# Kernel tuning notes

Measured on AMD Instinct MI355X. Metric: run time of the kernel, lower is better.

Reference implementation:

```python
import jax, jax.numpy as jnp
import numpy as np

B, T, N_EMBED, HEAD = 512, 256, 384, 64
BLOCK = 256
SCALE = N_EMBED ** -0.5  # source scales by input-channel dim, not head_size


def setup_inputs() -> dict:
    key = jax.random.key(0)
    kx, kk, kq, kv = jax.random.split(key, 4)
    x = jax.random.normal(kx, (B, T, N_EMBED), dtype=jnp.float32)
    # torch Linear(n_embed, head_size, bias=False) weights, stored as (in, out)
    s = N_EMBED ** -0.5
    Wk = jax.random.normal(kk, (N_EMBED, HEAD), dtype=jnp.float32) * s
    Wq = jax.random.normal(kq, (N_EMBED, HEAD), dtype=jnp.float32) * s
    Wv = jax.random.normal(kv, (N_EMBED, HEAD), dtype=jnp.float32) * s
    return {"x": x, "Wk": Wk, "Wq": Wq, "Wv": Wv}


def reference(x, Wk, Wq, Wv):
    Bx, Tx, _ = x.shape
    K = jnp.einsum('btc,ch->bth', x, Wk)
    Q = jnp.einsum('btc,ch->bth', x, Wq)
    V = jnp.einsum('btc,ch->bth', x, Wv)
    scores = jnp.einsum('bth,bsh->bts', Q, K) * SCALE  # [B, T, T]
    causal = jnp.tril(jnp.ones((Tx, Tx), dtype=bool))
    scores = jnp.where(causal[None, :, :], scores, -jnp.inf)
    W = jax.nn.softmax(scores, axis=-1)
    # dropout is identity in eval mode (reference baseline is deterministic)
    out = jnp.einsum('bts,bsh->bth', W, V)
    return out
```

## Files before the change

kernel.cpp:

```cpp
#include <hip/hip_runtime.h>
#include <hip/hip_bf16.h>

#define B_  512
#define T_  256
#define C_  384
#define H_  64
#define SCALE_ 0.05103103630798287f

typedef float f32x4  __attribute__((ext_vector_type(4)));
typedef short bf16x8 __attribute__((ext_vector_type(8)));
typedef short bf16x4 __attribute__((ext_vector_type(4)));

__device__ __forceinline__ unsigned short f2bf(float f) {
    union { float f; unsigned u; } v; v.f = f;
    unsigned r = v.u + 0x7FFFu + ((v.u >> 16) & 1u);
    return (unsigned short)(r >> 16);
}

__device__ __forceinline__ unsigned cvt_pk_bf16(float lo, float hi) {
    unsigned r;
    asm("v_cvt_pk_bf16_f32 %0, %1, %2" : "=v"(r) : "v"(lo), "v"(hi));
    return r;
}

__device__ __forceinline__ int swz64(int row, int col) {
    return row * 64 + (((col >> 3) ^ (row & 7)) << 3) + (col & 7);
}

__global__ __launch_bounds__(1024, 4) void att_head_kernel(
    const float* __restrict__ x,  const float* __restrict__ Wk,
    const float* __restrict__ Wq, const float* __restrict__ Wv,
    float* __restrict__ out)
{
    __shared__ __align__(16) short smem[53760];
    short* const wst0 = smem;
    short* const wst1 = smem + 12288;
    short* const Ks   = smem;
    short* const Vt   = smem + 16384;
    short* const Pb   = smem + 33280;

    const int tid  = threadIdx.x;
    const int b    = blockIdx.x;
    const int w    = tid >> 6;
    const int lane = tid & 63;
    const int g    = lane >> 4;
    const int i    = lane & 15;
    const int rb   = 16 * w;

    const float* xb = x + (size_t)b * T_ * C_;
    const float* Wm[3] = { Wk, Wq, Wv };

    f32x4 accP[12];
    #pragma unroll
    for (int nb = 0; nb < 12; nb++) accP[nb] = f32x4{0.f, 0.f, 0.f, 0.f};

    const float* xrow = xb + (size_t)(rb + i) * C_ + g * 8;

    auto stageW = [&](int kc, short* buf) {
        #pragma unroll
        for (int m = 0; m < 3; m++) {
            const float* Wp = Wm[m] + (size_t)(kc + w * 4) * H_ + lane;
            bf16x4 pk;
            #pragma unroll
            for (int jj = 0; jj < 4; jj++) pk[jj] = (short)f2bf(Wp[jj * H_]);
            const int row = m * 64 + lane;
            const int k0  = w * 4;
            *(bf16x4*)&buf[row * 64 + (((k0 >> 3) ^ (row & 7)) << 3) + (k0 & 7)] = pk;
        }
    };

    float4 xr[2][4];
    #pragma unroll
    for (int ks = 0; ks < 2; ks++)
        #pragma unroll
        for (int h = 0; h < 2; h++)
            xr[0][ks * 2 + h] = *(const float4*)(xrow + ks * 32 + h * 4);
    stageW(0, wst0);
    asm volatile("s_waitcnt lgkmcnt(0)\n\ts_barrier" ::: "memory");

    #pragma unroll
    for (int j = 0; j < 6; j++) {
        const int par = j & 1;
        short* cur = par ? wst1 : wst0;
        if (j < 5) {
            #pragma unroll
            for (int ks = 0; ks < 2; ks++)
                #pragma unroll
                for (int h = 0; h < 2; h++)
                    xr[par ^ 1][ks * 2 + h] = *(const float4*)(xrow + (j + 1) * 64 + ks * 32 + h * 4);
            stageW((j + 1) * 64, par ? wst0 : wst1);
        }
        bf16x8 afs[2];
        #pragma unroll
        for (int ks = 0; ks < 2; ks++)
            #pragma unroll
            for (int h = 0; h < 2; h++) {
                const float4 v = xr[par][ks * 2 + h];
                afs[ks][h * 4 + 0] = (short)f2bf(v.x);
                afs[ks][h * 4 + 1] = (short)f2bf(v.y);
                afs[ks][h * 4 + 2] = (short)f2bf(v.z);
                afs[ks][h * 4 + 3] = (short)f2bf(v.w);
            }
        #pragma unroll
        for (int nb = 0; nb < 12; nb++) {
            #pragma unroll
            for (int ks = 0; ks < 2; ks++) {
                const int brow = nb * 16 + i;
                const bf16x8 bfr = *(const bf16x8*)&cur[brow * 64 + (((ks * 4 + g) ^ (i & 7)) << 3)];
                accP[nb] = __builtin_amdgcn_mfma_f32_16x16x32_bf16(afs[ks], bfr, accP[nb], 0, 0, 0);
            }
        }
        asm volatile("s_waitcnt lgkmcnt(0)\n\ts_barrier" ::: "memory");
    }

    #pragma unroll
    for (int nb = 0; nb < 4; nb++)
        #pragma unroll
        for (int r = 0; r < 4; r++)
            Ks[swz64(rb + 4 * g + r, 16 * nb + i)] = (short)f2bf(accP[4 + nb][r]);
    asm volatile("s_waitcnt lgkmcnt(0)" ::: "memory");
    bf16x8 qf[2];
    #pragma unroll
    for (int ks = 0; ks < 2; ks++)
        qf[ks] = *(const bf16x8*)&Ks[(rb + i) * 64 + (((4 * ks + g) ^ (i & 7)) << 3)];
    asm volatile("s_waitcnt lgkmcnt(0)" ::: "memory");
    #pragma unroll
    for (int nb = 0; nb < 4; nb++)
        #pragma unroll
        for (int r = 0; r < 4; r++)
            Ks[swz64(rb + 4 * g + r, 16 * nb + i)] = (short)f2bf(accP[nb][r]);
    #pragma unroll
    for (int nb = 0; nb < 4; nb++) {
        bf16x4 pk;
        #pragma unroll
        for (int r = 0; r < 4; r++) pk[r] = (short)f2bf(accP[8 + nb][r]);
        *(bf16x4*)&Vt[(16 * nb + i) * 264 + rb + 4 * g] = pk;
    }
    asm volatile("s_waitcnt lgkmcnt(0)\n\ts_barrier" ::: "memory");

    short* const myP = Pb + w * 1280;
    const float NEG_INF = -__builtin_inff();
    float mrun = NEG_INF, lrun = 0.f;
    f32x4 accO[4];
    #pragma unroll
    for (int ht = 0; ht < 4; ht++) accO[ht] = f32x4{0.f, 0.f, 0.f, 0.f};

    auto PVADD = [&](int bufsel, int ck) {
        const bf16x8 pf = *(const bf16x8*)&myP[bufsel * 640 + i * 40 + 8 * g];
        #pragma unroll
        for (int ht = 0; ht < 4; ht++) {
            const bf16x8 vf = *(const bf16x8*)&Vt[(16 * ht + i) * 264 + 32 * ck + 8 * g];
            accO[ht] = __builtin_amdgcn_mfma_f32_16x16x32_bf16(vf, pf, accO[ht], 0, 0, 0);
        }
    };

    const int npair = w >> 1;
    #pragma unroll
    for (int p = 0; p < 8; p++) {
        if (p <= npair) {
            f32x4 sA[2];
            sA[0] = f32x4{0.f, 0.f, 0.f, 0.f};
            sA[1] = f32x4{0.f, 0.f, 0.f, 0.f};
            #pragma unroll
            for (int s = 0; s < 2; s++) {
                const int nt = 2 * p + s;
                if (nt <= w) {
                    #pragma unroll
                    for (int ks = 0; ks < 2; ks++) {
                        const bf16x8 kfr = *(const bf16x8*)&Ks[(16 * nt + i) * 64 +
                                (((4 * ks + g) ^ (i & 7)) << 3)];
                        sA[s] = __builtin_amdgcn_mfma_f32_16x16x32_bf16(kfr, qf[ks], sA[s], 0, 0, 0);
                    }
                }
            }
            if (p > 0) PVADD((p - 1) & 1, p - 1);

            float mt = NEG_INF;
            #pragma unroll
            for (int s = 0; s < 2; s++)
                #pragma unroll
                for (int r = 0; r < 4; r++) {
                    const int kv = 16 * (2 * p + s) + 4 * g + r;
                    const bool ok = (2 * p + s <= w) && (kv <= rb + i);
                    const float v = ok ? sA[s][r] * SCALE_ : NEG_INF;
                    sA[s][r] = v;
                    mt = fmaxf(mt, v);
                }
            mt = fmaxf(mt, __shfl_xor(mt, 16, 64));
            mt = fmaxf(mt, __shfl_xor(mt, 32, 64));

            if (!__all(mt <= mrun + 8.0f)) {
                const float mnew = fmaxf(mrun, mt);
                const float f = __expf(mrun - mnew);
                mrun = mnew; lrun *= f;
                #pragma unroll
                for (int ht = 0; ht < 4; ht++)
                    #pragma unroll
                    for (int r = 0; r < 4; r++) accO[ht][r] *= f;
            }
            #pragma unroll
            for (int s = 0; s < 2; s++) {
                const float p0 = __expf(sA[s][0] - mrun);
                const float p1 = __expf(sA[s][1] - mrun);
                const float p2 = __expf(sA[s][2] - mrun);
                const float p3 = __expf(sA[s][3] - mrun);
                lrun += (p0 + p1) + (p2 + p3);
                union { bf16x4 v; unsigned u[2]; } pk;
                pk.u[0] = cvt_pk_bf16(p0, p1);
                pk.u[1] = cvt_pk_bf16(p2, p3);
                *(bf16x4*)&myP[(p & 1) * 640 + i * 40 + 16 * s + 4 * g] = pk.v;
            }
        }
    }
    PVADD(npair & 1, npair);

    lrun += __shfl_xor(lrun, 16, 64);
    lrun += __shfl_xor(lrun, 32, 64);
    const float inv = 1.f / lrun;

    float* orow = out + ((size_t)b * T_ + rb + i) * H_;
    #pragma unroll
    for (int ht = 0; ht < 4; ht++) {
        float4 o;
        o.x = accO[ht][0] * inv;
        o.y = accO[ht][1] * inv;
        o.z = accO[ht][2] * inv;
        o.w = accO[ht][3] * inv;
        *(float4*)&orow[16 * ht + 4 * g] = o;
    }
}

extern "C" void kernel_launch(void* const* d_in, const int* in_sizes, int n_in,
                              void* d_out, int out_size, void* d_ws, size_t ws_size,
                              hipStream_t stream) {
    const float* x  = (const float*)d_in[0];
    const float* Wk = (const float*)d_in[1];
    const float* Wq = (const float*)d_in[2];
    const float* Wv = (const float*)d_in[3];
    float* out = (float*)d_out;
    (void)d_ws; (void)ws_size; (void)in_sizes; (void)n_in; (void)out_size;
    att_head_kernel<<<dim3(B_), dim3(1024), 0, stream>>>(x, Wk, Wq, Wv, out);
}
```

Baseline: 57.49 us.

## Retile QKV projection as 32x96 warp tiles with split-K prefetch and Q in LDS

The projection GEMM is re-tiled so each wave computes a 32-row by 96-column tile instead of 16 rows by all 192 columns. Each W fragment read from LDS now feeds two MFMAs, which halves B-operand LDS traffic per MFMA. The x prefetch is split into half-chunks to cut register pressure, and the conversion uses the packed bf16 instruction. Because Q is now spread across waves, it is staged through a new Q buffer in LDS. This raises shared memory use and adds an extra round trip for Q.

```diff
diff --git a/kernel.cpp b/kernel.cpp
--- a/kernel.cpp
+++ b/kernel.cpp
@@ -32,12 +32,13 @@
     const float* __restrict__ Wq, const float* __restrict__ Wv,
     float* __restrict__ out)
 {
-    __shared__ __align__(16) short smem[53760];
+    __shared__ __align__(16) short smem[78336];
     short* const wst0 = smem;
     short* const wst1 = smem + 12288;
-    short* const Ks   = smem;
-    short* const Vt   = smem + 16384;
-    short* const Pb   = smem + 33280;
+    short* const Qs   = smem;
+    short* const Ks   = smem + 24576;
+    short* const Vt   = smem + 40960;
+    short* const Pb   = smem + 57856;
 
     const int tid  = threadIdx.x;
     const int b    = blockIdx.x;
@@ -45,16 +46,20 @@
     const int lane = tid & 63;
     const int g    = lane >> 4;
     const int i    = lane & 15;
-    const int rb   = 16 * w;
+    const int wr   = w >> 1;
+    const int wc   = w & 1;
 
     const float* xb = x + (size_t)b * T_ * C_;
     const float* Wm[3] = { Wk, Wq, Wv };
 
-    f32x4 accP[12];
-    #pragma unroll
-    for (int nb = 0; nb < 12; nb++) accP[nb] = f32x4{0.f, 0.f, 0.f, 0.f};
-
-    const float* xrow = xb + (size_t)(rb + i) * C_ + g * 8;
+    f32x4 accP[2][6];
+    #pragma unroll
+    for (int s = 0; s < 2; s++)
+        #pragma unroll
+        for (int nb = 0; nb < 6; nb++) accP[s][nb] = f32x4{0.f, 0.f, 0.f, 0.f};
+
+    const float* xs0 = xb + (size_t)(32 * wr + i) * C_ + g * 8;
+    const float* xs1 = xs0 + 16 * C_;
 
     auto stageW = [&](int kc, short* buf) {
         #pragma unroll
@@ -69,74 +74,77 @@
         }
     };
 
-    float4 xr[2][4];
-    #pragma unroll
-    for (int ks = 0; ks < 2; ks++)
-        #pragma unroll
-        for (int h = 0; h < 2; h++)
-            xr[0][ks * 2 + h] = *(const float4*)(xrow + ks * 32 + h * 4);
+    float4 xr[2][2];
+    auto loadXhalf = [&](int j, int h) {
+        xr[0][0] = *(const float4*)(xs0 + 64 * j + 32 * h);
+        xr[0][1] = *(const float4*)(xs0 + 64 * j + 32 * h + 4);
+        xr[1][0] = *(const float4*)(xs1 + 64 * j + 32 * h);
+        xr[1][1] = *(const float4*)(xs1 + 64 * j + 32 * h + 4);
+    };
+
+    loadXhalf(0, 0);
     stageW(0, wst0);
     asm volatile("s_waitcnt lgkmcnt(0)\n\ts_barrier" ::: "memory");
 
     #pragma unroll
     for (int j = 0; j < 6; j++) {
-        const int par = j & 1;
-        short* cur = par ? wst1 : wst0;
-        if (j < 5) {
-            #pragma unroll
-            for (int ks = 0; ks < 2; ks++)
-                #pragma unroll
-                for (int h = 0; h < 2; h++)
-                    xr[par ^ 1][ks * 2 + h] = *(const float4*)(xrow + (j + 1) * 64 + ks * 32 + h * 4);
-            stageW((j + 1) * 64, par ? wst0 : wst1);
-        }
-        bf16x8 afs[2];
-        #pragma unroll
-        for (int ks = 0; ks < 2; ks++)
-            #pragma unroll
-            for (int h = 0; h < 2; h++) {
-                const float4 v = xr[par][ks * 2 + h];
-                afs[ks][h * 4 + 0] = (short)f2bf(v.x);
-                afs[ks][h * 4 + 1] = (short)f2bf(v.y);
-                afs[ks][h * 4 + 2] = (short)f2bf(v.z);
-                afs[ks][h * 4 + 3] = (short)f2bf(v.w);
-            }
-        #pragma unroll
-        for (int nb = 0; nb < 12; nb++) {
-            #pragma unroll
-            for (int ks = 0; ks < 2; ks++) {
-                const int brow = nb * 16 + i;
-                const bf16x8 bfr = *(const bf16x8*)&cur[brow * 64 + (((ks * 4 + g) ^ (i & 7)) << 3)];
-                accP[nb] = __builtin_amdgcn_mfma_f32_16x16x32_bf16(afs[ks], bfr, accP[nb], 0, 0, 0);
+        short* const cur = (j & 1) ? wst1 : wst0;
+        short* const alt = (j & 1) ? wst0 : wst1;
+        #pragma unroll
+        for (int h = 0; h < 2; h++) {
+            bf16x8 afs[2];
+            #pragma unroll
+            for (int s = 0; s < 2; s++) {
+                union { bf16x8 v; unsigned u[4]; } a;
+                a.u[0] = cvt_pk_bf16(xr[s][0].x, xr[s][0].y);
+                a.u[1] = cvt_pk_bf16(xr[s][0].z, xr[s][0].w);
+                a.u[2] = cvt_pk_bf16(xr[s][1].x, xr[s][1].y);
+                a.u[3] = cvt_pk_bf16(xr[s][1].z, xr[s][1].w);
+                afs[s] = a.v;
+            }
+            if (!(j == 5 && h == 1)) loadXhalf(j + (h & 1), h ^ 1);
+            if (h == 0 && j < 5) stageW((j + 1) * 64, alt);
+            #pragma unroll
+            for (int nb = 0; nb < 6; nb++) {
+                const int brow = 96 * wc + 16 * nb + i;
+                const bf16x8 bfr = *(const bf16x8*)&cur[brow * 64 +
+                        (((4 * h + g) ^ (i & 7)) << 3)];
+                accP[0][nb] = __builtin_amdgcn_mfma_f32_16x16x32_bf16(afs[0], bfr, accP[0][nb], 0, 0, 0);
+                accP[1][nb] = __builtin_amdgcn_mfma_f32_16x16x32_bf16(afs[1], bfr, accP[1][nb], 0, 0, 0);
             }
         }
         asm volatile("s_waitcnt lgkmcnt(0)\n\ts_barrier" ::: "memory");
     }
 
     #pragma unroll
-    for (int nb = 0; nb < 4; nb++)
-        #pragma unroll
-        for (int r = 0; r < 4; r++)
-            Ks[swz64(rb + 4 * g + r, 16 * nb + i)] = (short)f2bf(accP[4 + nb][r]);
-    asm volatile("s_waitcnt lgkmcnt(0)" ::: "memory");
+    for (int s = 0; s < 2; s++) {
+        const int row0 = 32 * wr + 16 * s + 4 * g;
+        #pragma unroll
+        for (int nb = 0; nb < 6; nb++) {
+            const int gc = 96 * wc + 16 * nb;
+            if (gc < 64) {
+                #pragma unroll
+                for (int r = 0; r < 4; r++)
+                    Ks[swz64(row0 + r, gc + i)] = (short)f2bf(accP[s][nb][r]);
+            } else if (gc < 128) {
+                #pragma unroll
+                for (int r = 0; r < 4; r++)
+                    Qs[swz64(row0 + r, gc - 64 + i)] = (short)f2bf(accP[s][nb][r]);
+            } else {
+                bf16x4 pk;
+                #pragma unroll
+                for (int r = 0; r < 4; r++) pk[r] = (short)f2bf(accP[s][nb][r]);
+                *(bf16x4*)&Vt[(gc - 128 + i) * 264 + row0] = pk;
+            }
+        }
+    }
+    asm volatile("s_waitcnt lgkmcnt(0)\n\ts_barrier" ::: "memory");
+
+    const int rb = 16 * w;
     bf16x8 qf[2];
     #pragma unroll
     for (int ks = 0; ks < 2; ks++)
-        qf[ks] = *(const bf16x8*)&Ks[(rb + i) * 64 + (((4 * ks + g) ^ (i & 7)) << 3)];
-    asm volatile("s_waitcnt lgkmcnt(0)" ::: "memory");
-    #pragma unroll
-    for (int nb = 0; nb < 4; nb++)
-        #pragma unroll
-        for (int r = 0; r < 4; r++)
-            Ks[swz64(rb + 4 * g + r, 16 * nb + i)] = (short)f2bf(accP[nb][r]);
-    #pragma unroll
-    for (int nb = 0; nb < 4; nb++) {
-        bf16x4 pk;
-        #pragma unroll
-        for (int r = 0; r < 4; r++) pk[r] = (short)f2bf(accP[8 + nb][r]);
-        *(bf16x4*)&Vt[(16 * nb + i) * 264 + rb + 4 * g] = pk;
-    }
-    asm volatile("s_waitcnt lgkmcnt(0)\n\ts_barrier" ::: "memory");
+        qf[ks] = *(const bf16x8*)&Qs[(rb + i) * 64 + (((4 * ks + g) ^ (i & 7)) << 3)];
 
     short* const myP = Pb + w * 1280;
     const float NEG_INF = -__builtin_inff();
```

Result: slower. 78.96 us (+37.3%).

## Build P operand in registers via permlane swaps instead of LDS round-trip

Applied to the files above, without the earlier changes.

Replaces the per-wave LDS staging buffer for softmax probabilities with an in-register transpose: v_permlane32_swap plus shuffles rearrange the packed bf16 P values into the MFMA B-operand layout. The PV MFMA now runs in the same iteration instead of being software-pipelined one step behind. LDS use shrinks (which may help occupancy) and LDS write/read traffic and waits disappear. In exchange it adds cross-lane shuffle instructions and drops the overlap the deferred PV update gave.

```diff
diff --git a/kernel.cpp b/kernel.cpp
--- a/kernel.cpp
+++ b/kernel.cpp
@@ -16,13 +16,11 @@
     unsigned r = v.u + 0x7FFFu + ((v.u >> 16) & 1u);
     return (unsigned short)(r >> 16);
 }
-
 __device__ __forceinline__ unsigned cvt_pk_bf16(float lo, float hi) {
     unsigned r;
     asm("v_cvt_pk_bf16_f32 %0, %1, %2" : "=v"(r) : "v"(lo), "v"(hi));
     return r;
 }
-
 __device__ __forceinline__ int swz64(int row, int col) {
     return row * 64 + (((col >> 3) ^ (row & 7)) << 3) + (col & 7);
 }
@@ -32,12 +30,11 @@
     const float* __restrict__ Wq, const float* __restrict__ Wv,
     float* __restrict__ out)
 {
-    __shared__ __align__(16) short smem[53760];
+    __shared__ __align__(16) short smem[33280];
     short* const wst0 = smem;
     short* const wst1 = smem + 12288;
     short* const Ks   = smem;
     short* const Vt   = smem + 16384;
-    short* const Pb   = smem + 33280;
 
     const int tid  = threadIdx.x;
     const int b    = blockIdx.x;
@@ -138,22 +135,13 @@
     }
     asm volatile("s_waitcnt lgkmcnt(0)\n\ts_barrier" ::: "memory");
 
-    short* const myP = Pb + w * 1280;
     const float NEG_INF = -__builtin_inff();
     float mrun = NEG_INF, lrun = 0.f;
     f32x4 accO[4];
     #pragma unroll
     for (int ht = 0; ht < 4; ht++) accO[ht] = f32x4{0.f, 0.f, 0.f, 0.f};
 
-    auto PVADD = [&](int bufsel, int ck) {
-        const bf16x8 pf = *(const bf16x8*)&myP[bufsel * 640 + i * 40 + 8 * g];
-        #pragma unroll
-        for (int ht = 0; ht < 4; ht++) {
-            const bf16x8 vf = *(const bf16x8*)&Vt[(16 * ht + i) * 264 + 32 * ck + 8 * g];
-            accO[ht] = __builtin_amdgcn_mfma_f32_16x16x32_bf16(vf, pf, accO[ht], 0, 0, 0);
-        }
-    };
-
+    const bool godd = (g & 1) != 0;
     const int npair = w >> 1;
     #pragma unroll
     for (int p = 0; p < 8; p++) {
@@ -173,8 +161,6 @@
                     }
                 }
             }
-            if (p > 0) PVADD((p - 1) & 1, p - 1);
-
             float mt = NEG_INF;
             #pragma unroll
             for (int s = 0; s < 2; s++)
@@ -198,21 +184,36 @@
                     #pragma unroll
                     for (int r = 0; r < 4; r++) accO[ht][r] *= f;
             }
-            #pragma unroll
-            for (int s = 0; s < 2; s++) {
-                const float p0 = __expf(sA[s][0] - mrun);
-                const float p1 = __expf(sA[s][1] - mrun);
-                const float p2 = __expf(sA[s][2] - mrun);
-                const float p3 = __expf(sA[s][3] - mrun);
-                lrun += (p0 + p1) + (p2 + p3);
-                union { bf16x4 v; unsigned u[2]; } pk;
-                pk.u[0] = cvt_pk_bf16(p0, p1);
-                pk.u[1] = cvt_pk_bf16(p2, p3);
-                *(bf16x4*)&myP[(p & 1) * 640 + i * 40 + 16 * s + 4 * g] = pk.v;
-            }
-        }
-    }
-    PVADD(npair & 1, npair);
+            float e0[4], e1[4];
+            #pragma unroll
+            for (int r = 0; r < 4; r++) {
+                e0[r] = __expf(sA[0][r] - mrun);
+                e1[r] = __expf(sA[1][r] - mrun);
+                lrun += e0[r] + e1[r];
+            }
+            unsigned a0 = cvt_pk_bf16(e0[0], e0[1]);
+            unsigned a1 = cvt_pk_bf16(e0[2], e0[3]);
+            unsigned b0 = cvt_pk_bf16(e1[0], e1[1]);
+            unsigned b1 = cvt_pk_bf16(e1[2], e1[3]);
+            asm volatile("v_permlane32_swap_b32 %0, %1" : "+v"(a0), "+v"(b0));
+            asm volatile("v_permlane32_swap_b32 %0, %1" : "+v"(a1), "+v"(b1));
+            const unsigned sa0 = __shfl_xor(a0, 16, 64);
+            const unsigned sa1 = __shfl_xor(a1, 16, 64);
+            const unsigned sb0 = __shfl_xor(b0, 16, 64);
+            const unsigned sb1 = __shfl_xor(b1, 16, 64);
+            union { bf16x8 v; unsigned u[4]; } pfB;
+            pfB.u[0] = godd ? sb0 : a0;
+            pfB.u[1] = godd ? sb1 : a1;
+            pfB.u[2] = godd ? b0  : sa0;
+            pfB.u[3] = godd ? b1  : sa1;
+
+            #pragma unroll
+            for (int ht = 0; ht < 4; ht++) {
+                const bf16x8 vf = *(const bf16x8*)&Vt[(16 * ht + i) * 264 + 32 * p + 8 * g];
+                accO[ht] = __builtin_amdgcn_mfma_f32_16x16x32_bf16(vf, pfB.v, accO[ht], 0, 0, 0);
+            }
+        }
+    }
 
     lrun += __shfl_xor(lrun, 16, 64);
     lrun += __shfl_xor(lrun, 32, 64);
```

New measurement: 59.09 us. +2.8%, slower.

## Stage all projection weights to LDS upfront, dropping per-chunk barriers

Applied to the files above, without the earlier changes.

Converts and stores all six K-chunks of the bf16 weights into LDS before the projection loop, using a register double-buffer for the global loads and packed bf16 conversion. The QKV projection loop then runs without the per-iteration barrier, keeping only one barrier at the end. This removes five workgroup barriers and the interleaving of weight staging with MFMA work. In exchange LDS use grows to about 144KB and the weight loads are exposed upfront instead of overlapped with compute.

```diff
diff --git a/kernel.cpp b/kernel.cpp
--- a/kernel.cpp
+++ b/kernel.cpp
@@ -16,13 +16,11 @@
     unsigned r = v.u + 0x7FFFu + ((v.u >> 16) & 1u);
     return (unsigned short)(r >> 16);
 }
-
 __device__ __forceinline__ unsigned cvt_pk_bf16(float lo, float hi) {
     unsigned r;
     asm("v_cvt_pk_bf16_f32 %0, %1, %2" : "=v"(r) : "v"(lo), "v"(hi));
     return r;
 }
-
 __device__ __forceinline__ int swz64(int row, int col) {
     return row * 64 + (((col >> 3) ^ (row & 7)) << 3) + (col & 7);
 }
@@ -32,12 +30,10 @@
     const float* __restrict__ Wq, const float* __restrict__ Wv,
     float* __restrict__ out)
 {
-    __shared__ __align__(16) short smem[53760];
-    short* const wst0 = smem;
-    short* const wst1 = smem + 12288;
-    short* const Ks   = smem;
-    short* const Vt   = smem + 16384;
-    short* const Pb   = smem + 33280;
+    __shared__ __align__(16) short smem[73728];
+    short* const Ks = smem;
+    short* const Vt = smem + 16384;
+    short* const Pb = smem + 33280;
 
     const int tid  = threadIdx.x;
     const int b    = blockIdx.x;
@@ -56,39 +52,57 @@
 
     const float* xrow = xb + (size_t)(rb + i) * C_ + g * 8;
 
-    auto stageW = [&](int kc, short* buf) {
-        #pragma unroll
-        for (int m = 0; m < 3; m++) {
-            const float* Wp = Wm[m] + (size_t)(kc + w * 4) * H_ + lane;
-            bf16x4 pk;
-            #pragma unroll
-            for (int jj = 0; jj < 4; jj++) pk[jj] = (short)f2bf(Wp[jj * H_]);
-            const int row = m * 64 + lane;
-            const int k0  = w * 4;
-            *(bf16x4*)&buf[row * 64 + (((k0 >> 3) ^ (row & 7)) << 3) + (k0 & 7)] = pk;
-        }
-    };
-
+    {
+        float wfa[12], wfb[12];
+        auto loadWchunk = [&](int j, float* dst) {
+            #pragma unroll
+            for (int m = 0; m < 3; m++) {
+                const float* Wp = Wm[m] + (size_t)(j * 64 + w * 4) * H_ + lane;
+                #pragma unroll
+                for (int jj = 0; jj < 4; jj++) dst[m * 4 + jj] = Wp[jj * H_];
+            }
+        };
+        auto writeWchunk = [&](int j, const float* src) {
+            short* buf = smem + j * 12288;
+            #pragma unroll
+            for (int m = 0; m < 3; m++) {
+                union { unsigned u; short s[2]; } p0, p1;
+                p0.u = cvt_pk_bf16(src[4 * m + 0], src[4 * m + 1]);
+                p1.u = cvt_pk_bf16(src[4 * m + 2], src[4 * m + 3]);
+                bf16x4 pk;
+                pk[0] = p0.s[0]; pk[1] = p0.s[1]; pk[2] = p1.s[0]; pk[3] = p1.s[1];
+                const int row = m * 64 + lane;
+                const int k0  = w * 4;
+                *(bf16x4*)&buf[row * 64 + (((k0 >> 3) ^ (row & 7)) << 3) + (k0 & 7)] = pk;
+            }
+        };
+        loadWchunk(0, wfa);
+        #pragma unroll
+        for (int j = 0; j < 6; j++) {
+            float* curW = (j & 1) ? wfb : wfa;
+            float* nxtW = (j & 1) ? wfa : wfb;
+            if (j < 5) loadWchunk(j + 1, nxtW);
+            writeWchunk(j, curW);
+        }
+    }
     float4 xr[2][4];
     #pragma unroll
     for (int ks = 0; ks < 2; ks++)
         #pragma unroll
         for (int h = 0; h < 2; h++)
             xr[0][ks * 2 + h] = *(const float4*)(xrow + ks * 32 + h * 4);
-    stageW(0, wst0);
     asm volatile("s_waitcnt lgkmcnt(0)\n\ts_barrier" ::: "memory");
 
     #pragma unroll
     for (int j = 0; j < 6; j++) {
         const int par = j & 1;
-        short* cur = par ? wst1 : wst0;
+        const short* cur = smem + j * 12288;
         if (j < 5) {
             #pragma unroll
             for (int ks = 0; ks < 2; ks++)
                 #pragma unroll
                 for (int h = 0; h < 2; h++)
                     xr[par ^ 1][ks * 2 + h] = *(const float4*)(xrow + (j + 1) * 64 + ks * 32 + h * 4);
-            stageW((j + 1) * 64, par ? wst0 : wst1);
         }
         bf16x8 afs[2];
         #pragma unroll
@@ -110,8 +124,8 @@
                 accP[nb] = __builtin_amdgcn_mfma_f32_16x16x32_bf16(afs[ks], bfr, accP[nb], 0, 0, 0);
             }
         }
-        asm volatile("s_waitcnt lgkmcnt(0)\n\ts_barrier" ::: "memory");
-    }
+    }
+    asm volatile("s_waitcnt lgkmcnt(0)\n\ts_barrier" ::: "memory");
 
     #pragma unroll
     for (int nb = 0; nb < 4; nb++)
```

Result: no change. 56.89 us (-1.1%).
